# Kernel optimization log

Hardware: AMD Instinct MI355X
Metric: run time of the kernel (lower is better)

Reference implementation:

```python
import jax, jax.numpy as jnp
import numpy as np

EMBED_DIM = 1024
NUM_HEADS = 16
HEAD_DIM = EMBED_DIM // NUM_HEADS


def setup_inputs() -> dict:
    key = jax.random.key(0)
    ks = jax.random.split(key, 11)
    B, N, C = 2, 2048, EMBED_DIM
    s = 1.0 / np.sqrt(C)
    return {
        "query": jax.random.normal(ks[0], (B, N, C), jnp.float32),
        "key": jax.random.normal(ks[1], (B, N, C), jnp.float32),
        "value": jax.random.normal(ks[2], (B, N, C), jnp.float32),
        # torch nn.Linear weights: [out_features, in_features]
        "Wq": jax.random.normal(ks[3], (C, C), jnp.float32) * s,
        "bq": jnp.zeros((C,), jnp.float32),
        "Wk": jax.random.normal(ks[4], (C, C), jnp.float32) * s,
        "bk": jnp.zeros((C,), jnp.float32),
        "Wv": jax.random.normal(ks[5], (C, C), jnp.float32) * s,
        "bv": jnp.zeros((C,), jnp.float32),
        "Wo": jax.random.normal(ks[6], (C, C), jnp.float32) * s,
        "bo": jnp.zeros((C,), jnp.float32),
    }


def reference(query, key, value, Wq, bq, Wk, bk, Wv, bv, Wo, bo):
    B, N, C = query.shape
    H, D = NUM_HEADS, HEAD_DIM
    # projections (torch Linear: x @ W.T + b)
    q = query @ Wq.T + bq
    k = key @ Wk.T + bk
    v = value @ Wv.T + bv
    # [B, N, C] -> [B, H, N, D]
    q = q.reshape(B, N, H, D).transpose(0, 2, 1, 3)
    k = k.reshape(B, N, H, D).transpose(0, 2, 1, 3)
    v = v.reshape(B, N, H, D).transpose(0, 2, 1, 3)
    # scores: [B, H, N, N]
    scores = jnp.einsum("bhqd,bhkd->bhqk", q, k) / jnp.sqrt(jnp.asarray(D, q.dtype))
    attn = jax.nn.softmax(scores, axis=-1)
    # attend: [B, H, N, D] -> [B, N, C]
    out = jnp.einsum("bhqk,bhkd->bhqd", attn, v)
    out = out.transpose(0, 2, 1, 3).reshape(B, N, C)
    return out @ Wo.T + bo
```

## Files before the change

### kernel.cpp

```cpp
#include <hip/hip_runtime.h>
#include <hip/hip_bf16.h>
#include <cstdint>

typedef short bf16x8 __attribute__((ext_vector_type(8)));
typedef float f32x4 __attribute__((ext_vector_type(4)));
typedef float f32x16 __attribute__((ext_vector_type(16)));
typedef uint32_t u32x4v __attribute__((ext_vector_type(4)));
typedef unsigned short u16;

#define BATCH 2
#define NTOK 2048
#define CDIM 1024
#define NHEAD 16
#define DHEAD 64
#define MROWS 4096
#define KDIM 1024
#define KVB 64
#define NT (NTOK / KVB)

__device__ __forceinline__ u16 f2bf(float x) {
    uint32_t b = __float_as_uint(x);
    uint32_t r = (b + 0x7fffu + ((b >> 16) & 1u)) >> 16;
    return (u16)r;
}

__device__ __forceinline__ uint32_t packbf2(float lo, float hi) {
    float2 f; f.x = lo; f.y = hi;
    __hip_bfloat162 h = __float22bfloat162_rn(f);
    uint32_t r;
    __builtin_memcpy(&r, &h, 4);
    return r;
}

__device__ __forceinline__ void gload_lds16(const void* g, void* l) {
    __builtin_amdgcn_global_load_lds((const __attribute__((address_space(1))) void*)g,
                                     (__attribute__((address_space(3))) void*)l,
                                     16, 0, 0);
}

__global__ __launch_bounds__(256) void cast_kernel(
    const float* __restrict__ q, const float* __restrict__ k, const float* __restrict__ v,
    const float* __restrict__ wq, const float* __restrict__ wk, const float* __restrict__ wv,
    const float* __restrict__ wo, u16* __restrict__ dst) {
    const size_t TOT = 16u << 20;
    size_t i0 = ((size_t)blockIdx.x * 256 + threadIdx.x) * 4;
    size_t stride = (size_t)gridDim.x * 256 * 4;
    for (size_t i = i0; i < TOT; i += stride) {
        const float* src;
        size_t off = i;
        if (i < (4u << 20))        { src = q;  }
        else if (i < (8u << 20))   { src = k;  off = i - (4u << 20); }
        else if (i < (12u << 20))  { src = v;  off = i - (8u << 20); }
        else if (i < (13u << 20))  { src = wq; off = i - (12u << 20); }
        else if (i < (14u << 20))  { src = wk; off = i - (13u << 20); }
        else if (i < (15u << 20))  { src = wv; off = i - (14u << 20); }
        else                       { src = wo; off = i - (15u << 20); }
        float4 f = *(const float4*)(src + off);
        u16 o0 = f2bf(f.x), o1 = f2bf(f.y), o2 = f2bf(f.z), o3 = f2bf(f.w);
        uint2 packed;
        packed.x = (uint32_t)o0 | ((uint32_t)o1 << 16);
        packed.y = (uint32_t)o2 | ((uint32_t)o3 << 16);
        *(uint2*)(dst + i) = packed;
    }
}

__global__ __launch_bounds__(256, 3) void gemm_qkv(
    const u16* __restrict__ Xq, const u16* __restrict__ Xk, const u16* __restrict__ Xv,
    const u16* __restrict__ Wq, const u16* __restrict__ Wk, const u16* __restrict__ Wv,
    const float* __restrict__ bq, const float* __restrict__ bk, const float* __restrict__ bv,
    u16* __restrict__ Qo, u16* __restrict__ Ko, u16* __restrict__ Vo) {
    __shared__ u16 sA[128 * 32];
    __shared__ u16 sB[128 * 32];
    const int tid = threadIdx.x;
    const int lane = tid & 63;
    const int wave = tid >> 6;
    const int z = blockIdx.z;
    const u16* A  = (z == 0) ? Xq : (z == 1) ? Xk : Xv;
    const u16* Bw = (z == 0) ? Wq : (z == 1) ? Wk : Wv;
    const float* bias = (z == 0) ? bq : (z == 1) ? bk : bv;
    u16* Out = (z == 0) ? Qo : (z == 1) ? Ko : Vo;
    const float scale = (z == 0) ? 0.125f : 1.0f;

    const int m0 = blockIdx.x * 128, n0 = blockIdx.y * 128;
    const int wm = (wave >> 1) * 64, wn = (wave & 1) * 64;
    f32x4 acc[4][4] = {};
    const int rsel = lane & 15;
    const int ksel = (lane >> 4) * 8;

    for (int k0 = 0; k0 < KDIM; k0 += 32) {
#pragma unroll
        for (int u = 0; u < 2; ++u) {
            int c = tid + u * 256;
            int row = c >> 2, cin = c & 3;
            gload_lds16(A + (size_t)(m0 + row) * KDIM + k0 + cin * 8, &sA[c * 8]);
            gload_lds16(Bw + (size_t)(n0 + row) * KDIM + k0 + cin * 8, &sB[c * 8]);
        }
        __syncthreads();
        bf16x8 af[4], bfr[4];
#pragma unroll
        for (int i = 0; i < 4; ++i)
            af[i] = *(const bf16x8*)&sA[(wm + i * 16 + rsel) * 32 + ksel];
#pragma unroll
        for (int j = 0; j < 4; ++j)
            bfr[j] = *(const bf16x8*)&sB[(wn + j * 16 + rsel) * 32 + ksel];
#pragma unroll
        for (int i = 0; i < 4; ++i)
#pragma unroll
            for (int j = 0; j < 4; ++j)
                acc[i][j] = __builtin_amdgcn_mfma_f32_16x16x32_bf16(af[i], bfr[j], acc[i][j], 0, 0, 0);
        __syncthreads();
    }

#pragma unroll
    for (int i = 0; i < 4; ++i) {
        int mbase = m0 + wm + i * 16 + (lane >> 4) * 4;
#pragma unroll
        for (int j = 0; j < 4; ++j) {
            int n = n0 + wn + j * 16 + (lane & 15);
            float bv2 = bias[n];
            int h = n >> 6, d = n & 63;
#pragma unroll
            for (int r = 0; r < 4; ++r) {
                int m = mbase + r;
                int b = m >> 11, tok = m & 2047;
                Out[(((size_t)(b * NHEAD + h)) * NTOK + tok) * DHEAD + d] =
                    f2bf((acc[i][j][r] + bv2) * scale);
            }
        }
    }
}

__global__ __launch_bounds__(256, 3) void gemm_out(
    const u16* __restrict__ A,
    const u16* __restrict__ Bw,
    const float* __restrict__ bias,
    float* __restrict__ Out,
    int M, int N, int K) {
    __shared__ u16 sA[128 * 32];
    __shared__ u16 sB[128 * 32];
    const int tid = threadIdx.x;
    const int lane = tid & 63;
    const int wave = tid >> 6;
    const int m0 = blockIdx.x * 128, n0 = blockIdx.y * 128;
    const int wm = (wave >> 1) * 64, wn = (wave & 1) * 64;
    f32x4 acc[4][4] = {};
    const int rsel = lane & 15;
    const int ksel = (lane >> 4) * 8;

    for (int k0 = 0; k0 < K; k0 += 32) {
#pragma unroll
        for (int u = 0; u < 2; ++u) {
            int c = tid + u * 256;
            int row = c >> 2, cin = c & 3;
            gload_lds16(A + (size_t)(m0 + row) * K + k0 + cin * 8, &sA[c * 8]);
            gload_lds16(Bw + (size_t)(n0 + row) * K + k0 + cin * 8, &sB[c * 8]);
        }
        __syncthreads();
        bf16x8 af[4], bfr[4];
#pragma unroll
        for (int i = 0; i < 4; ++i)
            af[i] = *(const bf16x8*)&sA[(wm + i * 16 + rsel) * 32 + ksel];
#pragma unroll
        for (int j = 0; j < 4; ++j)
            bfr[j] = *(const bf16x8*)&sB[(wn + j * 16 + rsel) * 32 + ksel];
#pragma unroll
        for (int i = 0; i < 4; ++i)
#pragma unroll
            for (int j = 0; j < 4; ++j)
                acc[i][j] = __builtin_amdgcn_mfma_f32_16x16x32_bf16(af[i], bfr[j], acc[i][j], 0, 0, 0);
        __syncthreads();
    }

#pragma unroll
    for (int i = 0; i < 4; ++i) {
        int mbase = m0 + wm + i * 16 + (lane >> 4) * 4;
#pragma unroll
        for (int j = 0; j < 4; ++j) {
            int n = n0 + wn + j * 16 + (lane & 15);
            float bv = bias[n];
#pragma unroll
            for (int r = 0; r < 4; ++r) {
                int m = mbase + r;
                Out[(size_t)m * N + n] = acc[i][j][r] + bv;
            }
        }
    }
}

__global__ __launch_bounds__(256, 2) void attn_kernel(
    const u16* __restrict__ Qg, const u16* __restrict__ Kg, const u16* __restrict__ Vg,
    u16* __restrict__ Og) {
    __shared__ u16 Ks[2][KVB * 64];
    __shared__ uint32_t Vt[2][64 * 32];
    const int tid = threadIdx.x, lane = tid & 63, wave = tid >> 6;
    const int hi = lane >> 5, lq = lane & 31;

    int flat = blockIdx.x;
    int vflat = (flat & 7) * 64 + (flat >> 3);
    int bh = vflat >> 4;
    int qtile = vflat & 15;

    const int h = bh & (NHEAD - 1), b = bh >> 4;
    const u16* Qh = Qg + (size_t)bh * NTOK * DHEAD;
    const u16* Kh = Kg + (size_t)bh * NTOK * DHEAD;
    const u16* Vh = Vg + (size_t)bh * NTOK * DHEAD;
    const int qrow0 = qtile * 128 + wave * 32;
    const int qr = qrow0 + lq;

    bf16x8 qf[4];
#pragma unroll
    for (int dk = 0; dk < 4; ++dk)
        qf[dk] = *(const bf16x8*)&Qh[(size_t)qr * DHEAD + dk * 16 + hi * 8];

    f32x16 acc0 = {}, acc1 = {};
    float mrun = -1e30f, lrun = 0.f;

    const int jp = tid & 31, od = tid >> 5;

    {
        const u16* vp = Vh + (size_t)(2 * jp) * DHEAD + od * 8;
        uint4 pva = *(const uint4*)vp;
        uint4 pvb = *(const uint4*)(vp + DHEAD);
#pragma unroll
        for (int u = 0; u < 2; ++u) {
            int c2 = tid + u * 256;
            int kv = c2 >> 3, gi = c2 & 7;
            gload_lds16(Kh + (size_t)kv * DHEAD + (gi ^ (kv & 7)) * 8, &Ks[0][c2 * 8]);
        }
        uint32_t aw[4] = {pva.x, pva.y, pva.z, pva.w};
        uint32_t bw[4] = {pvb.x, pvb.y, pvb.z, pvb.w};
        char* vn = (char*)&Vt[0][0];
#pragma unroll
        for (int i = 0; i < 8; ++i) {
            int d = od * 8 + i;
            uint32_t lo = (aw[i >> 1] >> ((i & 1) * 16)) & 0xffffu;
            uint32_t hi16 = (bw[i >> 1] >> ((i & 1) * 16)) & 0xffffu;
            *(uint32_t*)(vn + d * 128 + ((jp * 4) ^ ((d & 7) << 4))) = lo | (hi16 << 16);
        }
    }
    __syncthreads();

    int cur = 0;
    for (int t = 0; t < NT; ++t) {
        const bool pre = (t + 1 < NT);
        uint4 wva, wvb;
        if (pre) {
            const u16* vp = Vh + (size_t)((t + 1) * KVB + 2 * jp) * DHEAD + od * 8;
            wva = *(const uint4*)vp;
            wvb = *(const uint4*)(vp + DHEAD);
#pragma unroll
            for (int u = 0; u < 2; ++u) {
                int c2 = tid + u * 256;
                int kv = c2 >> 3, gi = c2 & 7;
                gload_lds16(Kh + (size_t)((t + 1) * KVB + kv) * DHEAD + (gi ^ (kv & 7)) * 8,
                            &Ks[cur ^ 1][c2 * 8]);
            }
        }

        f32x16 T0 = {}, T1 = {};
        const char* kb_ = (const char*)&Ks[cur][0];
#pragma unroll
        for (int dk = 0; dk < 4; ++dk) {
            int x = dk * 32 + hi * 16;
            int kv0 = lq, kv1 = 32 + lq;
            bf16x8 k0 = *(const bf16x8*)(kb_ + kv0 * 128 + (x ^ ((kv0 & 7) << 4)));
            bf16x8 k1 = *(const bf16x8*)(kb_ + kv1 * 128 + (x ^ ((kv1 & 7) << 4)));
            T0 = __builtin_amdgcn_mfma_f32_32x32x16_bf16(k0, qf[dk], T0, 0, 0, 0);
            T1 = __builtin_amdgcn_mfma_f32_32x32x16_bf16(k1, qf[dk], T1, 0, 0, 0);
        }

        float m16[16];
#pragma unroll
        for (int i = 0; i < 16; ++i) m16[i] = fmaxf(T0[i], T1[i]);
#pragma unroll
        for (int s2 = 8; s2 >= 1; s2 >>= 1)
#pragma unroll
            for (int i = 0; i < s2; ++i) m16[i] = fmaxf(m16[i], m16[i + s2]);
        float mx = fmaxf(m16[0], __shfl_xor(m16[0], 32));

        if (mx > mrun + 8.0f) {
            float scl = __expf(mrun - mx);
            mrun = mx;
            lrun *= scl;
            acc0 *= scl;
            acc1 *= scl;
        }

        float p0[16], p1[16];
#pragma unroll
        for (int i = 0; i < 16; ++i) { p0[i] = __expf(T0[i] - mrun); p1[i] = __expf(T1[i] - mrun); }
        float sm[16];
#pragma unroll
        for (int i = 0; i < 16; ++i) sm[i] = p0[i] + p1[i];
#pragma unroll
        for (int s2 = 8; s2 >= 1; s2 >>= 1)
#pragma unroll
            for (int i = 0; i < s2; ++i) sm[i] += sm[i + s2];
        lrun += sm[0] + __shfl_xor(sm[0], 32);

        bf16x8 pf[4];
        const bool hb = (hi != 0);
#pragma unroll
        for (int kb2 = 0; kb2 < 2; ++kb2) {
            const float* pp = kb2 ? p1 : p0;
#pragma unroll
            for (int hh = 0; hh < 2; ++hh) {
                int rb = hh * 8;
                uint32_t a0 = packbf2(pp[rb + 0], pp[rb + 1]);
                uint32_t a1 = packbf2(pp[rb + 2], pp[rb + 3]);
                uint32_t b0 = packbf2(pp[rb + 4], pp[rb + 5]);
                uint32_t b1 = packbf2(pp[rb + 6], pp[rb + 7]);
                uint32_t x0 = __shfl_xor(hb ? a0 : b0, 32);
                uint32_t x1 = __shfl_xor(hb ? a1 : b1, 32);
                uint32_t w0 = hb ? x0 : a0;
                uint32_t w1 = hb ? x1 : a1;
                uint32_t w2 = hb ? b0 : x0;
                uint32_t w3 = hb ? b1 : x1;
                u32x4v w = {w0, w1, w2, w3};
                pf[kb2 * 2 + hh] = *(bf16x8*)&w;
            }
        }

        const char* vb_ = (const char*)&Vt[cur][0];
#pragma unroll
        for (int db = 0; db < 2; ++db) {
            int d = db * 32 + lq;
#pragma unroll
            for (int ks = 0; ks < 4; ++ks) {
                int off = d * 128 + ((ks * 32 + hi * 16) ^ ((d & 7) << 4));
                bf16x8 vf = *(const bf16x8*)(vb_ + off);
                if (db == 0)
                    acc0 = __builtin_amdgcn_mfma_f32_32x32x16_bf16(vf, pf[ks], acc0, 0, 0, 0);
                else
                    acc1 = __builtin_amdgcn_mfma_f32_32x32x16_bf16(vf, pf[ks], acc1, 0, 0, 0);
            }
        }

        if (pre) {
            uint32_t aw[4] = {wva.x, wva.y, wva.z, wva.w};
            uint32_t bw[4] = {wvb.x, wvb.y, wvb.z, wvb.w};
            char* vn = (char*)&Vt[cur ^ 1][0];
#pragma unroll
            for (int i = 0; i < 8; ++i) {
                int d = od * 8 + i;
                uint32_t lo = (aw[i >> 1] >> ((i & 1) * 16)) & 0xffffu;
                uint32_t hi16 = (bw[i >> 1] >> ((i & 1) * 16)) & 0xffffu;
                *(uint32_t*)(vn + d * 128 + ((jp * 4) ^ ((d & 7) << 4))) = lo | (hi16 << 16);
            }
        }
        __syncthreads();
        cur ^= 1;
    }

    float rinv = 1.0f / lrun;
#pragma unroll
    for (int db = 0; db < 2; ++db) {
#pragma unroll
        for (int rq = 0; rq < 4; ++rq) {
            int based = db * 32 + 8 * rq + 4 * hi;
            float o0, o1, o2, o3;
            if (db == 0) {
                o0 = acc0[rq * 4 + 0]; o1 = acc0[rq * 4 + 1];
                o2 = acc0[rq * 4 + 2]; o3 = acc0[rq * 4 + 3];
            } else {
                o0 = acc1[rq * 4 + 0]; o1 = acc1[rq * 4 + 1];
                o2 = acc1[rq * 4 + 2]; o3 = acc1[rq * 4 + 3];
            }
            uint2 st;
            st.x = packbf2(o0 * rinv, o1 * rinv);
            st.y = packbf2(o2 * rinv, o3 * rinv);
            *(uint2*)&Og[((size_t)(b * NTOK + qr)) * CDIM + h * DHEAD + based] = st;
        }
    }
}

extern "C" void kernel_launch(void* const* d_in, const int* in_sizes, int n_in,
                              void* d_out, int out_size, void* d_ws, size_t ws_size,
                              hipStream_t stream) {
    const float* q  = (const float*)d_in[0];
    const float* k  = (const float*)d_in[1];
    const float* v  = (const float*)d_in[2];
    const float* Wq = (const float*)d_in[3];
    const float* bq = (const float*)d_in[4];
    const float* Wk = (const float*)d_in[5];
    const float* bk = (const float*)d_in[6];
    const float* Wv = (const float*)d_in[7];
    const float* bv = (const float*)d_in[8];
    const float* Wo = (const float*)d_in[9];
    const float* bo = (const float*)d_in[10];

    u16* wsp = (u16*)d_ws;
    u16* Xq  = wsp;
    u16* Xk  = Xq + (4u << 20);
    u16* Xv  = Xk + (4u << 20);
    u16* Wqb = Xv + (4u << 20);
    u16* Wkb = Wqb + (1u << 20);
    u16* Wvb = Wkb + (1u << 20);
    u16* Wob = Wvb + (1u << 20);
    u16* Qb  = Wob + (1u << 20);
    u16* Kb  = Qb + (4u << 20);
    u16* Vb  = Kb + (4u << 20);
    u16* Ab  = Xq;

    cast_kernel<<<2048, 256, 0, stream>>>(q, k, v, Wq, Wk, Wv, Wo, Xq);

    gemm_qkv<<<dim3(MROWS / 128, CDIM / 128, 3), 256, 0, stream>>>(
        Xq, Xk, Xv, Wqb, Wkb, Wvb, bq, bk, bv, Qb, Kb, Vb);

    attn_kernel<<<512, 256, 0, stream>>>(Qb, Kb, Vb, Ab);

    gemm_out<<<dim3(MROWS / 128, CDIM / 128), 256, 0, stream>>>(
        Ab, Wob, bo, (float*)d_out, MROWS, CDIM, KDIM);
}
```

Measured before the change: 141.5 us.

## Use exp2 softmax with folded log2e, permute K rows to drop P shuffles, add setprio

Folds log2(e) into the Q projection scale so the softmax can use the native exp2 instruction instead of __expf, and raises the lazy-rescale threshold to match base-2 units. K rows are loaded in a permuted order so the score accumulator layout already matches the P operand layout of the PV MFMA, which removes the cross-lane shuffles and selects used to repack P. MFMA sections are wrapped in s_setprio to favour matrix issue across waves. The risk is that the row permutation must line up exactly with the MFMA output layout, and the higher rescale threshold leaves less headroom in the unnormalised bf16 P values.

```diff
diff --git a/kernel.cpp b/kernel.cpp
--- a/kernel.cpp
+++ b/kernel.cpp
@@ -79,7 +79,7 @@
     const u16* Bw = (z == 0) ? Wq : (z == 1) ? Wk : Wv;
     const float* bias = (z == 0) ? bq : (z == 1) ? bk : bv;
     u16* Out = (z == 0) ? Qo : (z == 1) ? Ko : Vo;
-    const float scale = (z == 0) ? 0.125f : 1.0f;
+    const float scale = (z == 0) ? 0.125f * 1.44269504088896f : 1.0f;
 
     const int m0 = blockIdx.x * 128, n0 = blockIdx.y * 128;
     const int wm = (wave >> 1) * 64, wn = (wave & 1) * 64;
@@ -215,6 +215,8 @@
     f32x16 acc0 = {}, acc1 = {};
     float mrun = -1e30f, lrun = 0.f;
 
+    const int pr = ((lq >> 2) & 1) * 8 + (lq & 3) + ((lq >> 3) & 1) * 4 + (lq >> 4) * 16;
+
     const int jp = tid & 31, od = tid >> 5;
 
     {
@@ -259,15 +261,17 @@
 
         f32x16 T0 = {}, T1 = {};
         const char* kb_ = (const char*)&Ks[cur][0];
+        __builtin_amdgcn_s_setprio(1);
 #pragma unroll
         for (int dk = 0; dk < 4; ++dk) {
             int x = dk * 32 + hi * 16;
-            int kv0 = lq, kv1 = 32 + lq;
+            int kv0 = pr, kv1 = 32 + pr;
             bf16x8 k0 = *(const bf16x8*)(kb_ + kv0 * 128 + (x ^ ((kv0 & 7) << 4)));
             bf16x8 k1 = *(const bf16x8*)(kb_ + kv1 * 128 + (x ^ ((kv1 & 7) << 4)));
             T0 = __builtin_amdgcn_mfma_f32_32x32x16_bf16(k0, qf[dk], T0, 0, 0, 0);
             T1 = __builtin_amdgcn_mfma_f32_32x32x16_bf16(k1, qf[dk], T1, 0, 0, 0);
         }
+        __builtin_amdgcn_s_setprio(0);
 
         float m16[16];
 #pragma unroll
@@ -278,8 +282,8 @@
             for (int i = 0; i < s2; ++i) m16[i] = fmaxf(m16[i], m16[i + s2]);
         float mx = fmaxf(m16[0], __shfl_xor(m16[0], 32));
 
-        if (mx > mrun + 8.0f) {
-            float scl = __expf(mrun - mx);
+        if (mx > mrun + 11.0f) {
+            float scl = __builtin_amdgcn_exp2f(mrun - mx);
             mrun = mx;
             lrun *= scl;
             acc0 *= scl;
@@ -288,7 +292,10 @@
 
         float p0[16], p1[16];
 #pragma unroll
-        for (int i = 0; i < 16; ++i) { p0[i] = __expf(T0[i] - mrun); p1[i] = __expf(T1[i] - mrun); }
+        for (int i = 0; i < 16; ++i) {
+            p0[i] = __builtin_amdgcn_exp2f(T0[i] - mrun);
+            p1[i] = __builtin_amdgcn_exp2f(T1[i] - mrun);
+        }
         float sm[16];
 #pragma unroll
         for (int i = 0; i < 16; ++i) sm[i] = p0[i] + p1[i];
@@ -299,29 +306,22 @@
         lrun += sm[0] + __shfl_xor(sm[0], 32);
 
         bf16x8 pf[4];
-        const bool hb = (hi != 0);
 #pragma unroll
         for (int kb2 = 0; kb2 < 2; ++kb2) {
             const float* pp = kb2 ? p1 : p0;
 #pragma unroll
             for (int hh = 0; hh < 2; ++hh) {
                 int rb = hh * 8;
-                uint32_t a0 = packbf2(pp[rb + 0], pp[rb + 1]);
-                uint32_t a1 = packbf2(pp[rb + 2], pp[rb + 3]);
-                uint32_t b0 = packbf2(pp[rb + 4], pp[rb + 5]);
-                uint32_t b1 = packbf2(pp[rb + 6], pp[rb + 7]);
-                uint32_t x0 = __shfl_xor(hb ? a0 : b0, 32);
-                uint32_t x1 = __shfl_xor(hb ? a1 : b1, 32);
-                uint32_t w0 = hb ? x0 : a0;
-                uint32_t w1 = hb ? x1 : a1;
-                uint32_t w2 = hb ? b0 : x0;
-                uint32_t w3 = hb ? b1 : x1;
-                u32x4v w = {w0, w1, w2, w3};
+                u32x4v w = { packbf2(pp[rb + 0], pp[rb + 1]),
+                             packbf2(pp[rb + 2], pp[rb + 3]),
+                             packbf2(pp[rb + 4], pp[rb + 5]),
+                             packbf2(pp[rb + 6], pp[rb + 7]) };
                 pf[kb2 * 2 + hh] = *(bf16x8*)&w;
             }
         }
 
         const char* vb_ = (const char*)&Vt[cur][0];
+        __builtin_amdgcn_s_setprio(1);
 #pragma unroll
         for (int db = 0; db < 2; ++db) {
             int d = db * 32 + lq;
@@ -335,6 +335,7 @@
                     acc1 = __builtin_amdgcn_mfma_f32_32x32x16_bf16(vf, pf[ks], acc1, 0, 0, 0);
             }
         }
+        __builtin_amdgcn_s_setprio(0);
 
         if (pre) {
             uint32_t aw[4] = {wva.x, wva.y, wva.z, wva.w};
```

Result: faster. 137.8 us (-2.6%).
